# Optimization experiments

Hardware: AMD Instinct MI355X
Metric: run time of the kernel (lower is better)

Reference implementation:

```python
import jax, jax.numpy as jnp
import numpy as np

B, L, D = 2048, 200, 128
ITEM_D, USER_D, CAT_D, DUR_D = 64, 64, 32, 16
N_USERS, N_ITEMS, N_CAT, N_DUR = 100000, 100000, 1000, 10
UDENSE, IDENSE = 25, 3
CONCAT = USER_D + ITEM_D + CAT_D + DUR_D + UDENSE + IDENSE + D  # 332
MLP1, MLP2 = 256, 128


def setup_inputs() -> dict:
    key = jax.random.key(0)
    ks = jax.random.split(key, 24)
    f = jax.random.normal
    hist_table = 0.01 * f(ks[0], (N_ITEMS + 1, D), dtype=jnp.float32)
    hist_table = hist_table.at[0].set(0.0)  # padding_idx=0
    return {
        'user_id': jax.random.randint(ks[1], (B,), 0, N_USERS, dtype=jnp.int32),
        'item_id': jax.random.randint(ks[2], (B,), 0, N_ITEMS, dtype=jnp.int32),
        'item_category': jax.random.randint(ks[3], (B,), 0, N_CAT, dtype=jnp.int32),
        'item_dur_bkt': jax.random.randint(ks[4], (B,), 0, N_DUR, dtype=jnp.int32),
        'history_seq': jax.random.randint(ks[5], (B, L), 0, N_ITEMS + 1, dtype=jnp.int32),
        'user_dense': f(ks[6], (B, UDENSE), dtype=jnp.float32),
        'item_dense': f(ks[7], (B, IDENSE), dtype=jnp.float32),
        'user_table': 0.01 * f(ks[8], (N_USERS, USER_D), dtype=jnp.float32),
        'item_table': 0.01 * f(ks[9], (N_ITEMS, ITEM_D), dtype=jnp.float32),
        'cat_table': 0.01 * f(ks[10], (N_CAT, CAT_D), dtype=jnp.float32),
        'dur_table': 0.01 * f(ks[11], (N_DUR, DUR_D), dtype=jnp.float32),
        'hist_table': hist_table,
        'target_proj_W': f(ks[12], (D, ITEM_D), dtype=jnp.float32) / np.sqrt(ITEM_D).astype(np.float32),
        'gru_Wi': f(ks[13], (3 * D, D), dtype=jnp.float32) / np.sqrt(D).astype(np.float32),
        'gru_Wh': f(ks[14], (3 * D, D), dtype=jnp.float32) / np.sqrt(D).astype(np.float32),
        'gru_bi': jnp.zeros((3 * D,), jnp.float32),
        'gru_bh': jnp.zeros((3 * D,), jnp.float32),
        'au_Wr': f(ks[15], (D, 2 * D), dtype=jnp.float32) / np.sqrt(2 * D).astype(np.float32),
        'au_br': jnp.zeros((D,), jnp.float32),
        'au_Wu': f(ks[16], (D, 2 * D), dtype=jnp.float32) / np.sqrt(2 * D).astype(np.float32),
        'au_bu': jnp.zeros((D,), jnp.float32),
        'au_Wh': f(ks[17], (D, 2 * D), dtype=jnp.float32) / np.sqrt(2 * D).astype(np.float32),
        'au_bh': jnp.zeros((D,), jnp.float32),
        'mlp_W1': f(ks[18], (MLP1, CONCAT), dtype=jnp.float32) / np.sqrt(CONCAT).astype(np.float32),
        'mlp_b1': jnp.zeros((MLP1,), jnp.float32),
        'mlp_W2': f(ks[19], (MLP2, MLP1), dtype=jnp.float32) / np.sqrt(MLP1).astype(np.float32),
        'mlp_b2': jnp.zeros((MLP2,), jnp.float32),
        'mlp_W3': f(ks[20], (1, MLP2), dtype=jnp.float32) / np.sqrt(MLP2).astype(np.float32),
        'mlp_b3': jnp.zeros((1,), jnp.float32),
    }


def _dien_fwd(user_id, item_id, item_category, item_dur_bkt, history_seq,
              user_dense, item_dense, user_table, item_table, cat_table,
              dur_table, hist_table, target_proj_W, gru_Wi, gru_Wh, gru_bi,
              gru_bh, au_Wr, au_br, au_Wu, au_bu, au_Wh, au_bh,
              mlp_W1, mlp_b1, mlp_W2, mlp_b2, mlp_W3, mlp_b3):
    mask = history_seq > 0                      # (B, L) bool, True = real item
    hist_emb = hist_table[history_seq]          # (B, L, D)

    # ---- InterestExtractor: torch nn.GRU (eval mode, dropout off) ----
    gi = jnp.einsum('bld,ed->ble', hist_emb, gru_Wi) + gru_bi  # (B, L, 3D)

    def gru_step(h, gi_t):
        gh = h @ gru_Wh.T + gru_bh
        i_r, i_z, i_n = jnp.split(gi_t, 3, axis=-1)
        h_r, h_z, h_n = jnp.split(gh, 3, axis=-1)
        r = jax.nn.sigmoid(i_r + h_r)
        z = jax.nn.sigmoid(i_z + h_z)
        n = jnp.tanh(i_n + r * h_n)
        h_new = (1.0 - z) * n + z * h
        return h_new, h_new

    h0 = jnp.zeros((hist_emb.shape[0], D), hist_emb.dtype)
    _, hs = jax.lax.scan(gru_step, h0, jnp.swapaxes(gi, 0, 1))
    h_states = jnp.swapaxes(hs, 0, 1)           # (B, L, D)

    # ---- Target-aware attention scores ----
    i_emb = item_table[item_id]                  # (B, ITEM_D)
    target = i_emb @ target_proj_W.T             # (B, D)
    scores = jnp.einsum('bld,bd->bl', h_states, target) / np.float32(np.sqrt(D))
    scores = jnp.where(mask, scores, jnp.float32(-1e9))
    attn = jax.nn.softmax(scores, axis=-1)       # (B, L)

    # ---- InterestEvolving: AUGRU scan over L timesteps ----
    def augru_step(h, inputs):
        x_t, e_t, m_t = inputs                   # (B,D), (B,), (B,)
        comb = jnp.concatenate([x_t, h], axis=-1)
        r = jax.nn.sigmoid(comb @ au_Wr.T + au_br)
        u = jax.nn.sigmoid(comb @ au_Wu.T + au_bu)
        u_prime = e_t[:, None] * u
        h_tilde = jnp.tanh(jnp.concatenate([x_t, r * h], axis=-1) @ au_Wh.T + au_bh)
        h_new = (1.0 - u_prime) * h + u_prime * h_tilde
        valid = m_t[:, None].astype(h.dtype)
        return valid * h_new + (1.0 - valid) * h, None

    xs = (jnp.swapaxes(h_states, 0, 1), attn.T, mask.T)
    evolved, _ = jax.lax.scan(augru_step, jnp.zeros_like(h0), xs)  # (B, D)

    # ---- Final MLP head ----
    x = jnp.concatenate([
        user_table[user_id], i_emb, cat_table[item_category],
        dur_table[item_dur_bkt], user_dense, item_dense, evolved], axis=-1)
    h1 = jax.nn.relu(x @ mlp_W1.T + mlp_b1)
    h2 = jax.nn.relu(h1 @ mlp_W2.T + mlp_b2)
    logit = (h2 @ mlp_W3.T + mlp_b3)[:, 0]
    return jax.nn.sigmoid(logit)                 # (B,)


def reference(user_id, item_id, item_category, item_dur_bkt, history_seq,
              user_dense, item_dense, user_table, item_table, cat_table,
              dur_table, hist_table, target_proj_W, gru_Wi, gru_Wh, gru_bi,
              gru_bh, au_Wr, au_br, au_Wu, au_bu, au_Wh, au_bh,
              mlp_W1, mlp_b1, mlp_W2, mlp_b2, mlp_W3, mlp_b3):
    return _dien_fwd(user_id, item_id, item_category, item_dur_bkt, history_seq,
                     user_dense, item_dense, user_table, item_table, cat_table,
                     dur_table, hist_table, target_proj_W, gru_Wi, gru_Wh, gru_bi,
                     gru_bh, au_Wr, au_br, au_Wu, au_bu, au_Wh, au_bh,
                     mlp_W1, mlp_b1, mlp_W2, mlp_b2, mlp_W3, mlp_b3)
```

## Files before the change

kernel.cpp:

```cpp
#include <hip/hip_runtime.h>
#include <cstdint>
#include <cstddef>

#define BB    2048
#define LL    200
#define GR    8
#define MR    8

typedef __attribute__((ext_vector_type(4))) float f32x4;
typedef __attribute__((ext_vector_type(8))) short s16x8;

__device__ __forceinline__ float fastrcp(float x) { return __builtin_amdgcn_rcpf(x); }
__device__ __forceinline__ float sigmf(float x) { return fastrcp(1.f + __expf(-x)); }
__device__ __forceinline__ float tanh2(float x) {
    return __builtin_fmaf(2.f, fastrcp(1.f + __expf(-2.f * x)), -1.f);
}
__device__ __forceinline__ float dot4(float4 a, float4 b) {
    return a.x * b.x + a.y * b.y + a.z * b.z + a.w * b.w;
}
__device__ __forceinline__ float4 ld4(const float* p) { return *(const float4*)p; }

__device__ __forceinline__ unsigned short f2bf(float f) {
    union { float f; unsigned u; } v; v.f = f;
    unsigned r = (v.u + 0x7FFFu + ((v.u >> 16) & 1u)) >> 16;
    return (unsigned short)r;
}
__device__ __forceinline__ float bf2f(unsigned short b) {
    unsigned u = ((unsigned)b) << 16;
    union { unsigned u; float f; } v; v.u = u;
    return v.f;
}
__device__ __forceinline__ s16x8 pack8g(const float* p) {
    float4 a = ld4(p), b = ld4(p + 4);
    s16x8 o;
    o[0] = (short)f2bf(a.x); o[1] = (short)f2bf(a.y);
    o[2] = (short)f2bf(a.z); o[3] = (short)f2bf(a.w);
    o[4] = (short)f2bf(b.x); o[5] = (short)f2bf(b.y);
    o[6] = (short)f2bf(b.z); o[7] = (short)f2bf(b.w);
    return o;
}
#define MFMA(a, b, c) __builtin_amdgcn_mfma_f32_16x16x32_bf16((a), (b), (c), 0, 0, 0)

#define BAR() do { \
    asm volatile("s_waitcnt lgkmcnt(0)" ::: "memory"); \
    __builtin_amdgcn_sched_barrier(0); \
    __builtin_amdgcn_s_barrier(); \
    __builtin_amdgcn_sched_barrier(0); \
} while (0)

#define RED2(A, O0, O1) { \
    float s2_ = __shfl(A[2], srcl), s3_ = __shfl(A[3], srcl); \
    O0 = hi ? s2_ : A[0]; O1 = hi ? s3_ : A[1]; \
}

__global__ __launch_bounds__(256) void cvt_hist(const float* __restrict__ src,
                                                unsigned short* __restrict__ dst, int n8) {
    int i = blockIdx.x * 256 + threadIdx.x;
    if (i < n8) *(s16x8*)(dst + (size_t)i * 8) = pack8g(src + (size_t)i * 8);
}

__global__ void transpose_kernel(const float* __restrict__ src, float* __restrict__ dst,
                                 int rows, int cols) {
    int k = blockIdx.x;
    for (int j = threadIdx.x; j < rows; j += blockDim.x)
        dst[(size_t)k * rows + j] = src[(size_t)j * cols + k];
}

__global__ __launch_bounds__(128) void target_kernel(
    const int* __restrict__ item_id, const float* __restrict__ item_table,
    const float* __restrict__ projW, float* __restrict__ target) {
    __shared__ float ie[64];
    int b = blockIdx.x, d = threadIdx.x;
    if (d < 64) ie[d] = item_table[(size_t)item_id[b] * 64 + d];
    __syncthreads();
    float acc = 0.f;
    const float* w = projW + (size_t)d * 64;
#pragma unroll
    for (int k = 0; k < 64; k += 4) acc += dot4(ld4(&ie[k]), ld4(w + k));
    target[(size_t)b * 128 + d] = acc;
}

__global__ __launch_bounds__(512, 2) void gru_v9(
    const int* __restrict__ hseq, const unsigned short* __restrict__ hist_bf,
    const float* __restrict__ Wi, const float* __restrict__ Wh,
    const float* __restrict__ bi, const float* __restrict__ bh,
    unsigned short* __restrict__ h2) {
    __shared__ alignas(16) unsigned short hf[2][2048];
    __shared__ int sq[GR * LL];
    const int tid = threadIdx.x;
    const int w = tid >> 6, lane = tid & 63;
    const int b0 = blockIdx.x * GR;
    const int cb = (w << 4) | (lane & 15);
    const int kc_ = cb >> 5, kq_ = (cb >> 3) & 3, jj = cb & 7;
    const int srcl = lane & 31;
    const bool hi = lane >= 32;
    const int rowb = ((lane & 31) >> 4) * 4 + (hi ? 2 : 0);
    const int fs = ((tid >> 5) * 64 + ((tid >> 3) & 3) * 16 + (tid & 7)) * 8;
    const int xrow = lane & 7;
    const int xko = (lane >> 4) * 8;
    unsigned short* const h2p = h2 + (size_t)blockIdx.x * (LL * 1024);
    s16x8 wir[4], wiz[4], win[4], whr[4], whz[4], whn[4];
    {
        int c = lane & 15, kg = (lane >> 4) * 8;
#pragma unroll
        for (int kc = 0; kc < 4; ++kc) {
            int ko = kc * 32 + kg;
            wir[kc] = pack8g(Wi + (size_t)(w * 16 + c) * 128 + ko);
            wiz[kc] = pack8g(Wi + (size_t)(128 + w * 16 + c) * 128 + ko);
            win[kc] = pack8g(Wi + (size_t)(256 + w * 16 + c) * 128 + ko);
            whr[kc] = pack8g(Wh + (size_t)(w * 16 + c) * 128 + ko);
            whz[kc] = pack8g(Wh + (size_t)(128 + w * 16 + c) * 128 + ko);
            whn[kc] = pack8g(Wh + (size_t)(256 + w * 16 + c) * 128 + ko);
        }
    }
    const float b_r = bi[cb] + bh[cb];
    const float b_z = bi[128 + cb] + bh[128 + cb];
    const float bi_n = bi[256 + cb], bh_n = bh[256 + cb];
    float hold0 = 0.f, hold1 = 0.f;
    for (int i = tid; i < 2048; i += 512) { hf[0][i] = 0; hf[1][i] = 0; }
    for (int i = tid; i < GR * LL; i += 512)
        sq[i] = hseq[(size_t)(b0 + i / LL) * LL + i % LL];
    __syncthreads();

    s16x8 xA0, xA1, xA2, xA3, xB0, xB1, xB2, xB3;
    f32x4 xr, xz, xn;
#define XLOAD(TT, X0, X1, X2, X3) { \
    int idx_ = sq[xrow * LL + (TT)]; \
    const unsigned short* xp_ = hist_bf + ((size_t)idx_ << 7) + xko; \
    X0 = *(const s16x8*)(xp_);      X1 = *(const s16x8*)(xp_ + 32); \
    X2 = *(const s16x8*)(xp_ + 64); X3 = *(const s16x8*)(xp_ + 96); \
}
    XLOAD(0, xA0, xA1, xA2, xA3);
    xr = (f32x4){0, 0, 0, 0}; xz = xr; xn = xr;
    xr = MFMA(xA0, wir[0], xr); xz = MFMA(xA0, wiz[0], xz); xn = MFMA(xA0, win[0], xn);
    xr = MFMA(xA1, wir[1], xr); xz = MFMA(xA1, wiz[1], xz); xn = MFMA(xA1, win[1], xn);
    xr = MFMA(xA2, wir[2], xr); xz = MFMA(xA2, wiz[2], xz); xn = MFMA(xA2, win[2], xn);
    xr = MFMA(xA3, wir[3], xr); xz = MFMA(xA3, wiz[3], xz); xn = MFMA(xA3, win[3], xn);
    XLOAD(1, xB0, xB1, xB2, xB3);

#define GSTEP(TT, RD, XU0, XU1, XU2, XU3, XL0, XL1, XL2, XL3) { \
    const int tt = (TT); \
    if (tt > 0 && tid < 128) { \
        s16x8 hv = *(const s16x8*)&hf[RD][fs]; \
        *(s16x8*)(h2p + (unsigned)(tt - 1) * 1024 + tid * 8) = hv; \
    } \
    f32x4 ar = xr, az = xz, ain = xn; \
    f32x4 ahn = {0, 0, 0, 0}; \
    _Pragma("unroll") for (int kc = 0; kc < 4; ++kc) { \
        s16x8 ha = *(const s16x8*)&hf[RD][(kc * 64 + lane) * 8]; \
        ar = MFMA(ha, whr[kc], ar); az = MFMA(ha, whz[kc], az); ahn = MFMA(ha, whn[kc], ahn); \
    } \
    xr = (f32x4){0, 0, 0, 0}; xz = xr; xn = xr; \
    xr = MFMA(XU0, wir[0], xr); xz = MFMA(XU0, wiz[0], xz); xn = MFMA(XU0, win[0], xn); \
    xr = MFMA(XU1, wir[1], xr); xz = MFMA(XU1, wiz[1], xz); xn = MFMA(XU1, win[1], xn); \
    xr = MFMA(XU2, wir[2], xr); xz = MFMA(XU2, wiz[2], xz); xn = MFMA(XU2, win[2], xn); \
    xr = MFMA(XU3, wir[3], xr); xz = MFMA(XU3, wiz[3], xz); xn = MFMA(XU3, win[3], xn); \
    XLOAD(tt + 2 < LL ? tt + 2 : LL - 1, XL0, XL1, XL2, XL3); \
    { \
        float r0x, r1x, z0x, z1x, ni0, ni1, nh0, nh1; \
        RED2(ar, r0x, r1x); RED2(az, z0x, z1x); \
        RED2(ain, ni0, ni1); RED2(ahn, nh0, nh1); \
        float r0 = sigmf(r0x + b_r), z0 = sigmf(z0x + b_z); \
        float n0 = tanh2(ni0 + bi_n + r0 * (nh0 + bh_n)); \
        float hv0 = (1.f - z0) * n0 + z0 * hold0; hold0 = hv0; \
        hf[RD ^ 1][(kc_ * 64 + kq_ * 16 + rowb) * 8 + jj] = (short)f2bf(hv0); \
        float r1 = sigmf(r1x + b_r), z1 = sigmf(z1x + b_z); \
        float n1 = tanh2(ni1 + bi_n + r1 * (nh1 + bh_n)); \
        float hv1 = (1.f - z1) * n1 + z1 * hold1; hold1 = hv1; \
        hf[RD ^ 1][(kc_ * 64 + kq_ * 16 + rowb + 1) * 8 + jj] = (short)f2bf(hv1); \
    } \
    BAR(); \
}

    for (int t2 = 0; t2 < LL / 2; ++t2) {
        GSTEP(2 * t2,     0, xB0, xB1, xB2, xB3, xA0, xA1, xA2, xA3);
        GSTEP(2 * t2 + 1, 1, xA0, xA1, xA2, xA3, xB0, xB1, xB2, xB3);
    }
#undef GSTEP
#undef XLOAD
    if (tid < 128) {
        s16x8 hv = *(const s16x8*)&hf[0][fs];
        *(s16x8*)(h2p + (unsigned)(LL - 1) * 1024 + tid * 8) = hv;
    }
}

__global__ __launch_bounds__(512) void score_softmax2(
    const unsigned short* __restrict__ h2, const float* __restrict__ target,
    const int* __restrict__ hseq, float* __restrict__ attn) {
    __shared__ float tg[8][128];
    __shared__ float sA[8][LL];
    __shared__ float sB[8][LL];
    const int tid = threadIdx.x;
    const int blk = blockIdx.x;
    const int b0 = blk * 8;
    {
        int r = tid >> 6, d2 = (tid & 63) * 2;
        tg[r][d2] = target[(size_t)(b0 + r) * 128 + d2];
        tg[r][d2 + 1] = target[(size_t)(b0 + r) * 128 + d2 + 1];
    }
    __syncthreads();
    const unsigned short* const hp = h2 + (size_t)blk * (LL * 1024);
    const int g = tid >> 7;
    const int u = tid & 127;
    const int row = u & 7;
    const int d0 = (u >> 5) * 32 + ((u >> 3) & 3) * 8;
    const int half = u >> 6;
    for (int t = g; t < LL; t += 4) {
        s16x8 hv = *(const s16x8*)(hp + (unsigned)t * 1024 + u * 8);
        float acc = 0.f;
#pragma unroll
        for (int j = 0; j < 8; ++j)
            acc = __builtin_fmaf(bf2f((unsigned short)hv[j]), tg[row][d0 + j], acc);
        acc += __shfl_xor(acc, 8);
        acc += __shfl_xor(acc, 16);
        acc += __shfl_xor(acc, 32);
        if ((u & 63) < 8) { (half ? sB : sA)[row][t] = acc; }
    }
    __syncthreads();
    const int wv = tid >> 6, lane = tid & 63;
    float v[4];
#pragma unroll
    for (int m = 0; m < 4; ++m) {
        int t = lane + 64 * m;
        if (t < LL) {
            float s = (sA[wv][t] + sB[wv][t]) * 0.08838834764831845f;
            v[m] = (hseq[(size_t)(b0 + wv) * LL + t] > 0) ? s : -1e9f;
        } else
            v[m] = -3.0e38f;
    }
    float mx = fmaxf(fmaxf(v[0], v[1]), fmaxf(v[2], v[3]));
    for (int off = 1; off < 64; off <<= 1) mx = fmaxf(mx, __shfl_xor(mx, off));
    float s = 0.f;
#pragma unroll
    for (int m = 0; m < 4; ++m) {
        int t = lane + 64 * m;
        v[m] = (t < LL) ? __expf(v[m] - mx) : 0.f;
        s += v[m];
    }
    for (int off = 1; off < 64; off <<= 1) s += __shfl_xor(s, off);
    float inv = fastrcp(s);
#pragma unroll
    for (int m = 0; m < 4; ++m) {
        int t = lane + 64 * m;
        if (t < LL) attn[(size_t)(b0 + wv) * LL + t] = v[m] * inv;
    }
}

__global__ __launch_bounds__(512, 2) void augru_v9(
    const unsigned short* __restrict__ h2, const float* __restrict__ attn,
    const int* __restrict__ hseq,
    const float* __restrict__ Wr, const float* __restrict__ Wu,
    const float* __restrict__ Wht,
    const float* __restrict__ br, const float* __restrict__ bu,
    const float* __restrict__ bh, float* __restrict__ evolved) {
    __shared__ alignas(16) unsigned short hf[2][2048];
    __shared__ alignas(16) unsigned short rhf[2048];
    __shared__ float attl[GR * LL];
    const int tid = threadIdx.x;
    const int w = tid >> 6, lane = tid & 63;
    const int b0 = blockIdx.x * GR;
    const int cb = (w << 4) | (lane & 15);
    const int kc_ = cb >> 5, kq_ = (cb >> 3) & 3, jj = cb & 7;
    const int srcl = lane & 31;
    const bool hi = lane >= 32;
    const int rowb = ((lane & 31) >> 4) * 4 + (hi ? 2 : 0);
    const unsigned lofs = (unsigned)((lane >> 4) * 128 + (lane & 7) * 16);
    const char* const h2c = (const char*)(h2 + (size_t)blockIdx.x * (LL * 1024));
    s16x8 wr_[8], wu_[8], wx_[4], wh_[4];
    {
        int c = lane & 15, kg = (lane >> 4) * 8;
        int r0 = w * 16 + c;
#pragma unroll
        for (int kc = 0; kc < 8; ++kc) {
            wr_[kc] = pack8g(Wr + (size_t)r0 * 256 + kc * 32 + kg);
            wu_[kc] = pack8g(Wu + (size_t)r0 * 256 + kc * 32 + kg);
        }
#pragma unroll
        for (int kc = 0; kc < 4; ++kc) {
            wx_[kc] = pack8g(Wht + (size_t)r0 * 256 + kc * 32 + kg);
            wh_[kc] = pack8g(Wht + (size_t)r0 * 256 + 128 + kc * 32 + kg);
        }
    }
    const float br_c = br[cb], bu_c = bu[cb], bh_c = bh[cb];
    float hold0 = 0.f, hold1 = 0.f;
    for (int i = tid; i < 2048; i += 512) { hf[0][i] = 0; hf[1][i] = 0; rhf[i] = 0; }
    for (int i = tid; i < GR * LL; i += 512) {
        int r = i / LL, t = i % LL;
        float a = attn[(size_t)(b0 + r) * LL + t];
        attl[i] = (hseq[(size_t)(b0 + r) * LL + t] > 0) ? a : 0.f;
    }
    __syncthreads();

    s16x8 xA0, xA1, xA2, xA3, xB0, xB1, xB2, xB3;
    f32x4 xr, xu, xx;
#define XLOADA(TT, X0, X1, X2, X3) { \
    const char* xp_ = h2c + (unsigned)(TT) * 2048 + lofs; \
    X0 = *(const s16x8*)(xp_);        X1 = *(const s16x8*)(xp_ + 512); \
    X2 = *(const s16x8*)(xp_ + 1024); X3 = *(const s16x8*)(xp_ + 1536); \
}
    XLOADA(0, xA0, xA1, xA2, xA3);
    xr = (f32x4){0, 0, 0, 0}; xu = xr; xx = xr;
    xr = MFMA(xA0, wr_[0], xr); xu = MFMA(xA0, wu_[0], xu); xx = MFMA(xA0, wx_[0], xx);
    xr = MFMA(xA1, wr_[1], xr); xu = MFMA(xA1, wu_[1], xu); xx = MFMA(xA1, wx_[1], xx);
    xr = MFMA(xA2, wr_[2], xr); xu = MFMA(xA2, wu_[2], xu); xx = MFMA(xA2, wx_[2], xx);
    xr = MFMA(xA3, wr_[3], xr); xu = MFMA(xA3, wu_[3], xu); xx = MFMA(xA3, wx_[3], xx);
    XLOADA(1, xB0, xB1, xB2, xB3);

#define ASTEP(TT, RD, XU0, XU1, XU2, XU3, XL0, XL1, XL2, XL3) { \
    const int tt = (TT); \
    f32x4 ar = xr, au = xu, ax = xx; \
    _Pragma("unroll") for (int kc = 0; kc < 4; ++kc) { \
        s16x8 ha = *(const s16x8*)&hf[RD][(kc * 64 + lane) * 8]; \
        ar = MFMA(ha, wr_[kc + 4], ar); au = MFMA(ha, wu_[kc + 4], au); \
    } \
    xr = (f32x4){0, 0, 0, 0}; xu = xr; xx = xr; \
    xr = MFMA(XU0, wr_[0], xr); xu = MFMA(XU0, wu_[0], xu); xx = MFMA(XU0, wx_[0], xx); \
    xr = MFMA(XU1, wr_[1], xr); xu = MFMA(XU1, wu_[1], xu); xx = MFMA(XU1, wx_[1], xx); \
    xr = MFMA(XU2, wr_[2], xr); xu = MFMA(XU2, wu_[2], xu); xx = MFMA(XU2, wx_[2], xx); \
    xr = MFMA(XU3, wr_[3], xr); xu = MFMA(XU3, wu_[3], xu); xx = MFMA(XU3, wx_[3], xx); \
    XLOADA(tt + 2 < LL ? tt + 2 : LL - 1, XL0, XL1, XL2, XL3); \
    { \
        float a0, a1; \
        RED2(ar, a0, a1); \
        float r0 = sigmf(a0 + br_c), r1 = sigmf(a1 + br_c); \
        rhf[(kc_ * 64 + kq_ * 16 + rowb) * 8 + jj] = (short)f2bf(r0 * hold0); \
        rhf[(kc_ * 64 + kq_ * 16 + rowb + 1) * 8 + jj] = (short)f2bf(r1 * hold1); \
    } \
    BAR(); \
    f32x4 ah = {0, 0, 0, 0}; \
    _Pragma("unroll") for (int kc = 0; kc < 4; ++kc) { \
        s16x8 ra = *(const s16x8*)&rhf[(kc * 64 + lane) * 8]; \
        ah = MFMA(ra, wh_[kc], ah); \
    } \
    { \
        float u0, u1, t0, t1, g0, g1; \
        RED2(au, u0, u1); RED2(ax, t0, t1); RED2(ah, g0, g1); \
        float uu0 = sigmf(u0 + bu_c), uu1 = sigmf(u1 + bu_c); \
        float up0 = attl[rowb * LL + tt] * uu0; \
        float up1 = attl[(rowb + 1) * LL + tt] * uu1; \
        float ht0 = tanh2(t0 + g0 + bh_c), ht1 = tanh2(t1 + g1 + bh_c); \
        hold0 = (1.f - up0) * hold0 + up0 * ht0; \
        hold1 = (1.f - up1) * hold1 + up1 * ht1; \
        hf[RD ^ 1][(kc_ * 64 + kq_ * 16 + rowb) * 8 + jj] = (short)f2bf(hold0); \
        hf[RD ^ 1][(kc_ * 64 + kq_ * 16 + rowb + 1) * 8 + jj] = (short)f2bf(hold1); \
    } \
    BAR(); \
}

    for (int t2 = 0; t2 < LL / 2; ++t2) {
        ASTEP(2 * t2,     0, xB0, xB1, xB2, xB3, xA0, xA1, xA2, xA3);
        ASTEP(2 * t2 + 1, 1, xA0, xA1, xA2, xA3, xB0, xB1, xB2, xB3);
    }
#undef ASTEP
#undef XLOADA
    evolved[(size_t)(b0 + rowb) * 128 + cb] = hold0;
    evolved[(size_t)(b0 + rowb + 1) * 128 + cb] = hold1;
}

__global__ __launch_bounds__(256) void mlp_kernel(
    const int* __restrict__ user_id, const int* __restrict__ item_id,
    const int* __restrict__ item_cat, const int* __restrict__ item_dur,
    const float* __restrict__ user_dense, const float* __restrict__ item_dense,
    const float* __restrict__ user_table, const float* __restrict__ item_table,
    const float* __restrict__ cat_table, const float* __restrict__ dur_table,
    const float* __restrict__ evolved,
    const float* __restrict__ W1t, const float* __restrict__ b1,
    const float* __restrict__ W2t, const float* __restrict__ b2,
    const float* __restrict__ W3, const float* __restrict__ b3,
    float* __restrict__ out) {
    __shared__ float Xs[MR][332];
    __shared__ float h1s[MR][256];
    __shared__ float h2s[MR][128];
    __shared__ int ids[4][MR];
    const int tid = threadIdx.x;
    const int b0 = blockIdx.x * MR;
    if (tid < MR) {
        ids[0][tid] = user_id[b0 + tid];
        ids[1][tid] = item_id[b0 + tid];
        ids[2][tid] = item_cat[b0 + tid];
        ids[3][tid] = item_dur[b0 + tid];
    }
    __syncthreads();
    for (int i = tid; i < MR * 332; i += 256) {
        int r = i / 332, c = i % 332;
        int b = b0 + r;
        float v;
        if (c < 64) v = user_table[(size_t)ids[0][r] * 64 + c];
        else if (c < 128) v = item_table[(size_t)ids[1][r] * 64 + (c - 64)];
        else if (c < 160) v = cat_table[(size_t)ids[2][r] * 32 + (c - 128)];
        else if (c < 176) v = dur_table[(size_t)ids[3][r] * 16 + (c - 160)];
        else if (c < 201) v = user_dense[(size_t)b * 25 + (c - 176)];
        else if (c < 204) v = item_dense[(size_t)b * 3 + (c - 201)];
        else v = evolved[(size_t)b * 128 + (c - 204)];
        Xs[r][c] = v;
    }
    __syncthreads();
    {
        float acc[MR] = {0, 0, 0, 0, 0, 0, 0, 0};
        for (int k = 0; k < 332; ++k) {
            float ww = W1t[(size_t)k * 256 + tid];
#pragma unroll
            for (int r = 0; r < MR; ++r) acc[r] += Xs[r][k] * ww;
        }
        float bb = b1[tid];
#pragma unroll
        for (int r = 0; r < MR; ++r) h1s[r][tid] = fmaxf(acc[r] + bb, 0.f);
    }
    __syncthreads();
    if (tid < 128) {
        float acc[MR] = {0, 0, 0, 0, 0, 0, 0, 0};
        for (int k = 0; k < 256; ++k) {
            float ww = W2t[(size_t)k * 128 + tid];
#pragma unroll
            for (int r = 0; r < MR; ++r) acc[r] += h1s[r][k] * ww;
        }
        float bb = b2[tid];
#pragma unroll
        for (int r = 0; r < MR; ++r) h2s[r][tid] = fmaxf(acc[r] + bb, 0.f);
    }
    __syncthreads();
    {
        int r = tid >> 5, j = tid & 31;
        float p = 0.f;
#pragma unroll
        for (int m = 0; m < 4; ++m) p += h2s[r][j + 32 * m] * W3[j + 32 * m];
        p += __shfl_xor(p, 16);
        p += __shfl_xor(p, 8);
        p += __shfl_xor(p, 4);
        p += __shfl_xor(p, 2);
        p += __shfl_xor(p, 1);
        if (j == 0) out[b0 + r] = 1.f / (1.f + __expf(-(p + b3[0])));
    }
}

extern "C" void kernel_launch(void* const* d_in, const int* in_sizes, int n_in,
                              void* d_out, int out_size, void* d_ws, size_t ws_size,
                              hipStream_t stream) {
    const int* user_id = (const int*)d_in[0];
    const int* item_id = (const int*)d_in[1];
    const int* item_cat = (const int*)d_in[2];
    const int* item_dur = (const int*)d_in[3];
    const int* hseq = (const int*)d_in[4];
    const float* user_dense = (const float*)d_in[5];
    const float* item_dense = (const float*)d_in[6];
    const float* user_table = (const float*)d_in[7];
    const float* item_table = (const float*)d_in[8];
    const float* cat_table = (const float*)d_in[9];
    const float* dur_table = (const float*)d_in[10];
    const float* hist_table = (const float*)d_in[11];
    const float* projW = (const float*)d_in[12];
    const float* gWi = (const float*)d_in[13];
    const float* gWh = (const float*)d_in[14];
    const float* gbi = (const float*)d_in[15];
    const float* gbh = (const float*)d_in[16];
    const float* aWr = (const float*)d_in[17];
    const float* abr = (const float*)d_in[18];
    const float* aWu = (const float*)d_in[19];
    const float* abu = (const float*)d_in[20];
    const float* aWh = (const float*)d_in[21];
    const float* abh = (const float*)d_in[22];
    const float* mW1 = (const float*)d_in[23];
    const float* mb1 = (const float*)d_in[24];
    const float* mW2 = (const float*)d_in[25];
    const float* mb2 = (const float*)d_in[26];
    const float* mW3 = (const float*)d_in[27];
    const float* mb3 = (const float*)d_in[28];
    float* out = (float*)d_out;

    float* ws = (float*)d_ws;
    float* target = ws;
    unsigned short* h2 = (unsigned short*)(ws + 262144);
    float* attn = ws + 262144 + 26214400;
    float* evolved = attn + 409600;
    float* W1t = evolved + 262144;
    float* W2t = W1t + 84992;
    unsigned short* hist_bf = (unsigned short*)(W2t + 32768);

    const int n8 = 100001 * 16;
    hipLaunchKernelGGL(cvt_hist, dim3((n8 + 255) / 256), dim3(256), 0, stream,
                       hist_table, hist_bf, n8);
    hipLaunchKernelGGL(transpose_kernel, dim3(332), dim3(256), 0, stream, mW1, W1t, 256, 332);
    hipLaunchKernelGGL(transpose_kernel, dim3(256), dim3(128), 0, stream, mW2, W2t, 128, 256);
    hipLaunchKernelGGL(target_kernel, dim3(2048), dim3(128), 0, stream,
                       item_id, item_table, projW, target);
    hipLaunchKernelGGL(gru_v9, dim3(BB / GR), dim3(512), 0, stream,
                       hseq, hist_bf, gWi, gWh, gbi, gbh, h2);
    hipLaunchKernelGGL(score_softmax2, dim3(BB / 8), dim3(512), 0, stream,
                       h2, target, hseq, attn);
    hipLaunchKernelGGL(augru_v9, dim3(BB / GR), dim3(512), 0, stream,
                       h2, attn, hseq, aWr, aWu, aWh, abr, abu, abh, evolved);
    hipLaunchKernelGGL(mlp_kernel, dim3(BB / MR), dim3(256), 0, stream,
                       user_id, item_id, item_cat, item_dur, user_dense, item_dense,
                       user_table, item_table, cat_table, dur_table, evolved,
                       W1t, mb1, W2t, mb2, mW3, mb3, out);
}
```

Measured before the change: 464.6 us.

## Fuse attention scoring into GRU and softmax into AUGRU, removing score kernel

The GRU kernel now computes each hidden state's dot product with the target vector in-step via shuffle reductions and a small shared buffer, writing raw scaled scores. The softmax moves into the AUGRU prologue, so the separate score_softmax2 kernel, which re-read the whole h2 tensor, is removed. h2 is now stored in plain row-major layout with scalar 2-byte stores from each lane instead of vectorized copies, and the AUGRU load offsets are changed to match. This saves one full pass over h2 and a kernel launch, at the cost of extra shuffles and uncoalesced narrow stores inside the serial GRU loop.

```diff
diff --git a/kernel.cpp b/kernel.cpp
--- a/kernel.cpp
+++ b/kernel.cpp
@@ -80,12 +80,14 @@
     target[(size_t)b * 128 + d] = acc;
 }
 
-__global__ __launch_bounds__(512, 2) void gru_v9(
+__global__ __launch_bounds__(512, 2) void gru_v10(
     const int* __restrict__ hseq, const unsigned short* __restrict__ hist_bf,
     const float* __restrict__ Wi, const float* __restrict__ Wh,
     const float* __restrict__ bi, const float* __restrict__ bh,
-    unsigned short* __restrict__ h2) {
+    const float* __restrict__ target,
+    unsigned short* __restrict__ h2, float* __restrict__ scores) {
     __shared__ alignas(16) unsigned short hf[2][2048];
+    __shared__ float scoreb[2][64];
     __shared__ int sq[GR * LL];
     const int tid = threadIdx.x;
     const int w = tid >> 6, lane = tid & 63;
@@ -95,7 +97,6 @@
     const int srcl = lane & 31;
     const bool hi = lane >= 32;
     const int rowb = ((lane & 31) >> 4) * 4 + (hi ? 2 : 0);
-    const int fs = ((tid >> 5) * 64 + ((tid >> 3) & 3) * 16 + (tid & 7)) * 8;
     const int xrow = lane & 7;
     const int xko = (lane >> 4) * 8;
     unsigned short* const h2p = h2 + (size_t)blockIdx.x * (LL * 1024);
@@ -116,6 +117,8 @@
     const float b_r = bi[cb] + bh[cb];
     const float b_z = bi[128 + cb] + bh[128 + cb];
     const float bi_n = bi[256 + cb], bh_n = bh[256 + cb];
+    const float tg0 = target[(size_t)(b0 + rowb) * 128 + cb];
+    const float tg1 = target[(size_t)(b0 + rowb + 1) * 128 + cb];
     float hold0 = 0.f, hold1 = 0.f;
     for (int i = tid; i < 2048; i += 512) { hf[0][i] = 0; hf[1][i] = 0; }
     for (int i = tid; i < GR * LL; i += 512)
@@ -140,9 +143,10 @@
 
 #define GSTEP(TT, RD, XU0, XU1, XU2, XU3, XL0, XL1, XL2, XL3) { \
     const int tt = (TT); \
-    if (tt > 0 && tid < 128) { \
-        s16x8 hv = *(const s16x8*)&hf[RD][fs]; \
-        *(s16x8*)(h2p + (unsigned)(tt - 1) * 1024 + tid * 8) = hv; \
+    if (tt > 0 && lane == 16) {   \
+        float s = 0.f; \
+        _Pragma("unroll") for (int wv = 0; wv < 8; ++wv) s += scoreb[RD ^ 1][w * 8 + wv]; \
+        scores[(size_t)(b0 + w) * LL + tt - 1] = s * 0.08838834764831845f; \
     } \
     f32x4 ar = xr, az = xz, ain = xn; \
     f32x4 ahn = {0, 0, 0, 0}; \
@@ -163,11 +167,23 @@
         float r0 = sigmf(r0x + b_r), z0 = sigmf(z0x + b_z); \
         float n0 = tanh2(ni0 + bi_n + r0 * (nh0 + bh_n)); \
         float hv0 = (1.f - z0) * n0 + z0 * hold0; hold0 = hv0; \
-        hf[RD ^ 1][(kc_ * 64 + kq_ * 16 + rowb) * 8 + jj] = (short)f2bf(hv0); \
+        unsigned short hb0 = f2bf(hv0); \
+        h2p[(unsigned)tt * 1024 + rowb * 128 + cb] = hb0; \
+        hf[RD ^ 1][(kc_ * 64 + kq_ * 16 + rowb) * 8 + jj] = (short)hb0; \
         float r1 = sigmf(r1x + b_r), z1 = sigmf(z1x + b_z); \
         float n1 = tanh2(ni1 + bi_n + r1 * (nh1 + bh_n)); \
         float hv1 = (1.f - z1) * n1 + z1 * hold1; hold1 = hv1; \
-        hf[RD ^ 1][(kc_ * 64 + kq_ * 16 + rowb + 1) * 8 + jj] = (short)f2bf(hv1); \
+        unsigned short hb1 = f2bf(hv1); \
+        h2p[(unsigned)tt * 1024 + (rowb + 1) * 128 + cb] = hb1; \
+        hf[RD ^ 1][(kc_ * 64 + kq_ * 16 + rowb + 1) * 8 + jj] = (short)hb1; \
+        float p0 = hv0 * tg0, p1 = hv1 * tg1; \
+        _Pragma("unroll") for (int off = 1; off < 16; off <<= 1) { \
+            p0 += __shfl_xor(p0, off); p1 += __shfl_xor(p1, off); \
+        } \
+        if ((lane & 15) == 0) { \
+            scoreb[RD][rowb * 8 + w] = p0; \
+            scoreb[RD][(rowb + 1) * 8 + w] = p1; \
+        } \
     } \
     BAR(); \
 }
@@ -178,76 +194,16 @@
     }
 #undef GSTEP
 #undef XLOAD
-    if (tid < 128) {
-        s16x8 hv = *(const s16x8*)&hf[0][fs];
-        *(s16x8*)(h2p + (unsigned)(LL - 1) * 1024 + tid * 8) = hv;
-    }
-}
-
-__global__ __launch_bounds__(512) void score_softmax2(
-    const unsigned short* __restrict__ h2, const float* __restrict__ target,
-    const int* __restrict__ hseq, float* __restrict__ attn) {
-    __shared__ float tg[8][128];
-    __shared__ float sA[8][LL];
-    __shared__ float sB[8][LL];
-    const int tid = threadIdx.x;
-    const int blk = blockIdx.x;
-    const int b0 = blk * 8;
-    {
-        int r = tid >> 6, d2 = (tid & 63) * 2;
-        tg[r][d2] = target[(size_t)(b0 + r) * 128 + d2];
-        tg[r][d2 + 1] = target[(size_t)(b0 + r) * 128 + d2 + 1];
-    }
-    __syncthreads();
-    const unsigned short* const hp = h2 + (size_t)blk * (LL * 1024);
-    const int g = tid >> 7;
-    const int u = tid & 127;
-    const int row = u & 7;
-    const int d0 = (u >> 5) * 32 + ((u >> 3) & 3) * 8;
-    const int half = u >> 6;
-    for (int t = g; t < LL; t += 4) {
-        s16x8 hv = *(const s16x8*)(hp + (unsigned)t * 1024 + u * 8);
-        float acc = 0.f;
-#pragma unroll
-        for (int j = 0; j < 8; ++j)
-            acc = __builtin_fmaf(bf2f((unsigned short)hv[j]), tg[row][d0 + j], acc);
-        acc += __shfl_xor(acc, 8);
-        acc += __shfl_xor(acc, 16);
-        acc += __shfl_xor(acc, 32);
-        if ((u & 63) < 8) { (half ? sB : sA)[row][t] = acc; }
-    }
-    __syncthreads();
-    const int wv = tid >> 6, lane = tid & 63;
-    float v[4];
-#pragma unroll
-    for (int m = 0; m < 4; ++m) {
-        int t = lane + 64 * m;
-        if (t < LL) {
-            float s = (sA[wv][t] + sB[wv][t]) * 0.08838834764831845f;
-            v[m] = (hseq[(size_t)(b0 + wv) * LL + t] > 0) ? s : -1e9f;
-        } else
-            v[m] = -3.0e38f;
-    }
-    float mx = fmaxf(fmaxf(v[0], v[1]), fmaxf(v[2], v[3]));
-    for (int off = 1; off < 64; off <<= 1) mx = fmaxf(mx, __shfl_xor(mx, off));
-    float s = 0.f;
-#pragma unroll
-    for (int m = 0; m < 4; ++m) {
-        int t = lane + 64 * m;
-        v[m] = (t < LL) ? __expf(v[m] - mx) : 0.f;
-        s += v[m];
-    }
-    for (int off = 1; off < 64; off <<= 1) s += __shfl_xor(s, off);
-    float inv = fastrcp(s);
-#pragma unroll
-    for (int m = 0; m < 4; ++m) {
-        int t = lane + 64 * m;
-        if (t < LL) attn[(size_t)(b0 + wv) * LL + t] = v[m] * inv;
-    }
-}
-
-__global__ __launch_bounds__(512, 2) void augru_v9(
-    const unsigned short* __restrict__ h2, const float* __restrict__ attn,
+    if (lane == 16) {
+        float s = 0.f;
+#pragma unroll
+        for (int wv = 0; wv < 8; ++wv) s += scoreb[1][w * 8 + wv];
+        scores[(size_t)(b0 + w) * LL + LL - 1] = s * 0.08838834764831845f;
+    }
+}
+
+__global__ __launch_bounds__(512, 2) void augru_v10(
+    const unsigned short* __restrict__ h2, const float* __restrict__ scores,
     const int* __restrict__ hseq,
     const float* __restrict__ Wr, const float* __restrict__ Wu,
     const float* __restrict__ Wht,
@@ -264,7 +220,7 @@
     const int srcl = lane & 31;
     const bool hi = lane >= 32;
     const int rowb = ((lane & 31) >> 4) * 4 + (hi ? 2 : 0);
-    const unsigned lofs = (unsigned)((lane >> 4) * 128 + (lane & 7) * 16);
+    const unsigned lofs = (unsigned)((lane & 7) * 256 + (lane >> 4) * 16);
     const char* const h2c = (const char*)(h2 + (size_t)blockIdx.x * (LL * 1024));
     s16x8 wr_[8], wu_[8], wx_[4], wh_[4];
     {
@@ -284,10 +240,33 @@
     const float br_c = br[cb], bu_c = bu[cb], bh_c = bh[cb];
     float hold0 = 0.f, hold1 = 0.f;
     for (int i = tid; i < 2048; i += 512) { hf[0][i] = 0; hf[1][i] = 0; rhf[i] = 0; }
-    for (int i = tid; i < GR * LL; i += 512) {
-        int r = i / LL, t = i % LL;
-        float a = attn[(size_t)(b0 + r) * LL + t];
-        attl[i] = (hseq[(size_t)(b0 + r) * LL + t] > 0) ? a : 0.f;
+    {
+        float vv[4];
+#pragma unroll
+        for (int m = 0; m < 4; ++m) {
+            int t = lane + 64 * m;
+            if (t < LL) {
+                float s = scores[(size_t)(b0 + w) * LL + t];
+                vv[m] = (hseq[(size_t)(b0 + w) * LL + t] > 0) ? s : -1e9f;
+            } else
+                vv[m] = -3.0e38f;
+        }
+        float mx = fmaxf(fmaxf(vv[0], vv[1]), fmaxf(vv[2], vv[3]));
+        for (int off = 1; off < 64; off <<= 1) mx = fmaxf(mx, __shfl_xor(mx, off));
+        float ssum = 0.f;
+#pragma unroll
+        for (int m = 0; m < 4; ++m) {
+            int t = lane + 64 * m;
+            vv[m] = (t < LL) ? __expf(vv[m] - mx) : 0.f;
+            ssum += vv[m];
+        }
+        for (int off = 1; off < 64; off <<= 1) ssum += __shfl_xor(ssum, off);
+        float inv = fastrcp(ssum);
+#pragma unroll
+        for (int m = 0; m < 4; ++m) {
+            int t = lane + 64 * m;
+            if (t < LL) attl[w * LL + t] = vv[m] * inv;
+        }
     }
     __syncthreads();
 
@@ -295,8 +274,8 @@
     f32x4 xr, xu, xx;
 #define XLOADA(TT, X0, X1, X2, X3) { \
     const char* xp_ = h2c + (unsigned)(TT) * 2048 + lofs; \
-    X0 = *(const s16x8*)(xp_);        X1 = *(const s16x8*)(xp_ + 512); \
-    X2 = *(const s16x8*)(xp_ + 1024); X3 = *(const s16x8*)(xp_ + 1536); \
+    X0 = *(const s16x8*)(xp_);       X1 = *(const s16x8*)(xp_ + 64); \
+    X2 = *(const s16x8*)(xp_ + 128); X3 = *(const s16x8*)(xp_ + 192); \
 }
     XLOADA(0, xA0, xA1, xA2, xA3);
     xr = (f32x4){0, 0, 0, 0}; xu = xr; xx = xr;
@@ -470,8 +449,8 @@
     float* ws = (float*)d_ws;
     float* target = ws;
     unsigned short* h2 = (unsigned short*)(ws + 262144);
-    float* attn = ws + 262144 + 26214400;
-    float* evolved = attn + 409600;
+    float* scores = ws + 262144 + 26214400;
+    float* evolved = scores + 409600;
     float* W1t = evolved + 262144;
     float* W2t = W1t + 84992;
     unsigned short* hist_bf = (unsigned short*)(W2t + 32768);
@@ -483,12 +462,10 @@
     hipLaunchKernelGGL(transpose_kernel, dim3(256), dim3(128), 0, stream, mW2, W2t, 128, 256);
     hipLaunchKernelGGL(target_kernel, dim3(2048), dim3(128), 0, stream,
                        item_id, item_table, projW, target);
-    hipLaunchKernelGGL(gru_v9, dim3(BB / GR), dim3(512), 0, stream,
-                       hseq, hist_bf, gWi, gWh, gbi, gbh, h2);
-    hipLaunchKernelGGL(score_softmax2, dim3(BB / 8), dim3(512), 0, stream,
-                       h2, target, hseq, attn);
-    hipLaunchKernelGGL(augru_v9, dim3(BB / GR), dim3(512), 0, stream,
-                       h2, attn, hseq, aWr, aWu, aWh, abr, abu, abh, evolved);
+    hipLaunchKernelGGL(gru_v10, dim3(BB / GR), dim3(512), 0, stream,
+                       hseq, hist_bf, gWi, gWh, gbi, gbh, target, h2, scores);
+    hipLaunchKernelGGL(augru_v10, dim3(BB / GR), dim3(512), 0, stream,
+                       h2, scores, hseq, aWr, aWu, aWh, abr, abu, abh, evolved);
     hipLaunchKernelGGL(mlp_kernel, dim3(BB / MR), dim3(256), 0, stream,
                        user_id, item_id, item_cat, item_dur, user_dense, item_dense,
                        user_table, item_table, cat_table, dur_table, evolved,
```

New measurement: 493.0 us. +6.1%, slower.
